# Kernel optimization log

Measured on AMD Instinct MI355X. Metric: run time of the kernel, lower is better.

The kernel has to match this reference:

```python
import jax, jax.numpy as jnp
from jax import lax
import numpy as np

RANK = 128
INPUT_DIM = 128
OUT_DIM = 32
N = 128
L = 512
INIT_STD = 1.0 / np.sqrt(RANK * INPUT_DIM)  # variance-preserving recurrence


def setup_inputs() -> dict:
    key = jax.random.key(0)
    k_x, k_A, k_a, k_O = jax.random.split(key, 4)
    x = jax.random.normal(k_x, (N, L, INPUT_DIM), dtype=jnp.float32)
    A = INIT_STD * jax.random.normal(k_A, (RANK, INPUT_DIM, RANK), dtype=jnp.float32)
    alpha = INIT_STD * jax.random.normal(k_a, (RANK,), dtype=jnp.float32)
    Omega = INIT_STD * jax.random.normal(k_O, (RANK, OUT_DIM), dtype=jnp.float32)
    return {"x": x, "alpha": alpha, "A": A, "Omega": Omega}


def reference(x, alpha, A, Omega):
    # x: [N, L, D]; alpha: [R]; A: [R, D, R]; Omega: [R, M]
    # h_0 = einsum('i,ijk,nj->nk', alpha, A, x[:,0])
    h0 = jnp.einsum('i,ijk,nj->nk', alpha, A, x[:, 0, :])

    def step(h, xt):
        # h: [N, R], xt: [N, D] -> new h: [N, R]
        h = jnp.einsum('ni,ijk,nj->nk', h, A, xt)
        return h, None

    xs = jnp.swapaxes(x, 0, 1)[1:]  # [L-1, N, D]
    h, _ = lax.scan(step, h0, xs)
    out = jnp.einsum('ni,im->nm', h, Omega)  # [N, M]
    return jnp.squeeze(out)
```

## Files before the change

kernel.cpp:

```cpp
#include <hip/hip_runtime.h>

typedef _Float16 f16;
typedef _Float16 half8 __attribute__((ext_vector_type(8)));
typedef _Float16 half4v __attribute__((ext_vector_type(4)));
typedef float f32x4 __attribute__((ext_vector_type(4)));


__global__ void k_cvt_x(const float* __restrict__ in, f16* __restrict__ out) {
    int idx = blockIdx.x * blockDim.x + threadIdx.x;
    float4 v = ((const float4*)in)[idx];
    half4v o;
    o[0] = (f16)v.x; o[1] = (f16)v.y; o[2] = (f16)v.z; o[3] = (f16)v.w;
    ((half4v*)out)[idx] = o;
}

__global__ void k_cvt_A(const float* __restrict__ A, f16* __restrict__ Af2) {
    int o = blockIdx.x * blockDim.x + threadIdx.x;
    int i = o >> 14;
    int k = (o >> 7) & 127;
    int j = o & 127;
    Af2[o] = (f16)A[(i << 14) + (j << 7) + k];
}

__global__ __launch_bounds__(256, 2)
void k_gemm(const f16* __restrict__ Af2, const f16* __restrict__ Xh,
            f16* __restrict__ B, int t0, int logTc) {
    __shared__ f16 lA[128 * 128];
    __shared__ f16 lX[128 * 128];
    const int qtile = blockIdx.x;
    const int i = blockIdx.y;
    const int tid = threadIdx.x;
    const int row = tid >> 4;
    const int ch = tid & 15;
    const int Tcm1 = (1 << logTc) - 1;

    {
        const f16* srcA = Af2 + ((size_t)i << 14);
#pragma unroll
        for (int r = 0; r < 128; r += 16) {
            int rr = row + r;
            uint4 v = *(const uint4*)(srcA + (rr << 7) + (ch << 3));
            *(uint4*)(&lA[(rr << 7) + ((ch ^ (rr & 15)) << 3)]) = v;
        }
#pragma unroll
        for (int r = 0; r < 128; r += 16) {
            int rr = row + r;
            int qr = (qtile << 7) + rr;
            int n = qr >> logTc;
            int trel = qr & Tcm1;
            const f16* srcX = Xh + (((size_t)(n << 9) + t0 + trel) << 7);
            uint4 v = *(const uint4*)(srcX + (ch << 3));
            *(uint4*)(&lX[(rr << 7) + ((ch ^ (rr & 15)) << 3)]) = v;
        }
    }
    __syncthreads();

    const int wave = tid >> 6;
    const int lane = tid & 63;
    const int l15 = lane & 15;
    const int l4 = lane >> 4;
    f32x4 acc[8][2] = {};

#pragma unroll
    for (int ks = 0; ks < 4; ++ks) {
        const int c = (ks << 2) + l4;
        half8 afr[8], bfr[2];
#pragma unroll
        for (int mt = 0; mt < 8; ++mt) {
            int rowA = (mt << 4) + l15;
            afr[mt] = *(const half8*)(&lA[(rowA << 7) + ((c ^ l15) << 3)]);
        }
#pragma unroll
        for (int qt = 0; qt < 2; ++qt) {
            int rowX = (wave << 5) + (qt << 4) + l15;
            bfr[qt] = *(const half8*)(&lX[(rowX << 7) + ((c ^ l15) << 3)]);
        }
#pragma unroll
        for (int mt = 0; mt < 8; ++mt)
#pragma unroll
            for (int qt = 0; qt < 2; ++qt)
                acc[mt][qt] = __builtin_amdgcn_mfma_f32_16x16x32_f16(
                    afr[mt], bfr[qt], acc[mt][qt], 0, 0, 0);
    }

    __syncthreads();
    f16* stage = lA;
#pragma unroll
    for (int mt = 0; mt < 8; ++mt)
#pragma unroll
        for (int qt = 0; qt < 2; ++qt) {
            int q = (wave << 5) + (qt << 4) + l15;
            int chunk = (mt << 1) + (l4 >> 1);
            int hf = l4 & 1;
            half4v o;
            o[0] = (f16)acc[mt][qt][0];
            o[1] = (f16)acc[mt][qt][1];
            o[2] = (f16)acc[mt][qt][2];
            o[3] = (f16)acc[mt][qt][3];
            *(half4v*)(&stage[(q << 7) + (((chunk ^ l15) << 3) + (hf << 2))]) = o;
        }
    __syncthreads();
    {
        const int lr = lane >> 4;
        const int lc = lane & 15;
#pragma unroll
        for (int it = 0; it < 8; ++it) {
            int q = (wave << 5) + (it << 2) + lr;
            uint4 v = *(const uint4*)(&stage[(q << 7) + ((lc ^ (q & 15)) << 3)]);
            size_t qg = (size_t)((qtile << 7) + q);
            *(uint4*)(B + (qg << 14) + (i << 7) + (lc << 3)) = v;
        }
    }
}

__global__ __launch_bounds__(256, 1)
void k_chain(const f16* __restrict__ B, float* __restrict__ hstate,
             const float* __restrict__ alpha, const float* __restrict__ Om,
             float* __restrict__ out, int Tc, int first, int last) {
    __shared__ float hl[128];
    __shared__ float part[16][132];
    const int n = blockIdx.x;
    const int tid = threadIdx.x;
    const int kg = tid & 15;
    const int iq = tid >> 4;

    if (tid < 128) hl[tid] = first ? alpha[tid] : hstate[(n << 7) + tid];
    __syncthreads();

    const f16* bbase = B + (((size_t)n * Tc) << 14) + (iq << 10) + (kg << 3);
    half8 buf[4][8];
#pragma unroll
    for (int s = 0; s < 4; ++s)
#pragma unroll
        for (int ii = 0; ii < 8; ++ii)
            buf[s][ii] = *(const half8*)(bbase + ((size_t)s << 14) + (ii << 7));

    for (int t = 0; t < Tc; t += 4) {
#pragma unroll
        for (int s = 0; s < 4; ++s) {
            float4 h0 = *(const float4*)&hl[iq << 3];
            float4 h1 = *(const float4*)&hl[(iq << 3) + 4];
            float acc[8] = {0, 0, 0, 0, 0, 0, 0, 0};
#pragma unroll
            for (int ii = 0; ii < 4; ++ii) {
                float hv = (&h0.x)[ii];
#pragma unroll
                for (int j = 0; j < 8; ++j)
                    acc[j] += hv * (float)buf[s][ii][j];
            }
#pragma unroll
            for (int ii = 0; ii < 4; ++ii) {
                float hv = (&h1.x)[ii];
#pragma unroll
                for (int j = 0; j < 8; ++j)
                    acc[j] += hv * (float)buf[s][ii + 4][j];
            }
            int tn = t + s + 4;
            if (tn < Tc) {
#pragma unroll
                for (int ii = 0; ii < 8; ++ii)
                    buf[s][ii] = *(const half8*)(bbase + ((size_t)tn << 14) + (ii << 7));
            }
            *(float4*)(&part[iq][kg << 3])       = make_float4(acc[0], acc[1], acc[2], acc[3]);
            *(float4*)(&part[iq][(kg << 3) + 4]) = make_float4(acc[4], acc[5], acc[6], acc[7]);
            __syncthreads();
            if (tid < 128) {
                float s0 = part[0][tid] + part[1][tid];
                float s1 = part[2][tid] + part[3][tid];
                float s2 = part[4][tid] + part[5][tid];
                float s3 = part[6][tid] + part[7][tid];
                s0 += part[8][tid] + part[9][tid];
                s1 += part[10][tid] + part[11][tid];
                s2 += part[12][tid] + part[13][tid];
                s3 += part[14][tid] + part[15][tid];
                hl[tid] = (s0 + s1) + (s2 + s3);
            }
            __syncthreads();
        }
    }

    if (!last) {
        if (tid < 128) hstate[(n << 7) + tid] = hl[tid];
    } else if (tid < 32) {
        float s = 0.f;
        for (int i2 = 0; i2 < 128; ++i2) s += hl[i2] * Om[(i2 << 5) + tid];
        out[(n << 5) + tid] = s;
    }
}

extern "C" void kernel_launch(void* const* d_in, const int* in_sizes, int n_in,
                              void* d_out, int out_size, void* d_ws, size_t ws_size,
                              hipStream_t stream) {
    const float* x     = (const float*)d_in[0];
    const float* alpha = (const float*)d_in[1];
    const float* A     = (const float*)d_in[2];
    const float* Om    = (const float*)d_in[3];
    float* out = (float*)d_out;

    char* ws = (char*)d_ws;
    f16*   Af2    = (f16*)ws;
    f16*   Xh     = (f16*)(ws + ((size_t)4 << 20));
    float* hstate = (float*)(ws + ((size_t)20 << 20));
    f16*   Bc     = (f16*)(ws + ((size_t)21 << 20));

    int Tc = 32;
    while (Tc > 4 && ((size_t)21 << 20) + ((size_t)Tc << 22) > ws_size) Tc >>= 1;
    int logTc = 31 - __builtin_clz(Tc);
    int nch = 512 / Tc;

    k_cvt_x<<<8192, 256, 0, stream>>>(x, Xh);
    k_cvt_A<<<8192, 256, 0, stream>>>(A, Af2);

    for (int c = 0; c < nch; ++c) {
        k_gemm<<<dim3(Tc, 128), 256, 0, stream>>>(Af2, Xh, Bc, c * Tc, logTc);
        k_chain<<<128, 256, 0, stream>>>(Bc, hstate, alpha, Om, out,
                                         Tc, c == 0, c == nch - 1);
    }
    (void)in_sizes; (void)n_in; (void)out_size;
}
```

Measured before the change: 1.017 ms.

## Make GEMM blocks persistent over q-tiles, reusing A slice and prefetching X

The GEMM grid drops from Tc*128 blocks to 512 fixed blocks. Each block loads its A slice into LDS once and loops over Tc/4 q-tiles. The X tile for the next iteration is prefetched into registers while the current MFMA and store phase runs, and the staging buffer moves from lA to lX so A stays resident. This cuts redundant A loads and hides X load latency, at the cost of fewer blocks, more barriers per block, and extra register pressure from the prefetch buffer.

```diff
diff --git a/kernel.cpp b/kernel.cpp
--- a/kernel.cpp
+++ b/kernel.cpp
@@ -24,11 +24,12 @@
 
 __global__ __launch_bounds__(256, 2)
 void k_gemm(const f16* __restrict__ Af2, const f16* __restrict__ Xh,
-            f16* __restrict__ B, int t0, int logTc) {
+            f16* __restrict__ B, int t0, int logTc, int qtPerBlock) {
     __shared__ f16 lA[128 * 128];
     __shared__ f16 lX[128 * 128];
-    const int qtile = blockIdx.x;
-    const int i = blockIdx.y;
+    const int bx = blockIdx.x;
+    const int i = bx >> 2;
+    const int qt0 = bx & 3;
     const int tid = threadIdx.x;
     const int row = tid >> 4;
     const int ch = tid & 15;
@@ -42,74 +43,94 @@
             uint4 v = *(const uint4*)(srcA + (rr << 7) + (ch << 3));
             *(uint4*)(&lA[(rr << 7) + ((ch ^ (rr & 15)) << 3)]) = v;
         }
-#pragma unroll
-        for (int r = 0; r < 128; r += 16) {
-            int rr = row + r;
+    }
+
+    uint4 xr[8];
+    auto loadX = [&](int qtile) {
+#pragma unroll
+        for (int r = 0; r < 8; ++r) {
+            int rr = (r << 4) + row;
             int qr = (qtile << 7) + rr;
             int n = qr >> logTc;
             int trel = qr & Tcm1;
-            const f16* srcX = Xh + (((size_t)(n << 9) + t0 + trel) << 7);
-            uint4 v = *(const uint4*)(srcX + (ch << 3));
-            *(uint4*)(&lX[(rr << 7) + ((ch ^ (rr & 15)) << 3)]) = v;
-        }
-    }
+            xr[r] = *(const uint4*)(Xh + (((size_t)(n << 9) + t0 + trel) << 7) + (ch << 3));
+        }
+    };
+    auto xToLds = [&]() {
+#pragma unroll
+        for (int r = 0; r < 8; ++r) {
+            int rr = (r << 4) + row;
+            *(uint4*)(&lX[(rr << 7) + ((ch ^ (rr & 15)) << 3)]) = xr[r];
+        }
+    };
+
+    loadX(qt0);
+    xToLds();
     __syncthreads();
 
     const int wave = tid >> 6;
     const int lane = tid & 63;
     const int l15 = lane & 15;
     const int l4 = lane >> 4;
-    f32x4 acc[8][2] = {};
-
-#pragma unroll
-    for (int ks = 0; ks < 4; ++ks) {
-        const int c = (ks << 2) + l4;
-        half8 afr[8], bfr[2];
-#pragma unroll
-        for (int mt = 0; mt < 8; ++mt) {
-            int rowA = (mt << 4) + l15;
-            afr[mt] = *(const half8*)(&lA[(rowA << 7) + ((c ^ l15) << 3)]);
-        }
-#pragma unroll
-        for (int qt = 0; qt < 2; ++qt) {
-            int rowX = (wave << 5) + (qt << 4) + l15;
-            bfr[qt] = *(const half8*)(&lX[(rowX << 7) + ((c ^ l15) << 3)]);
-        }
+
+    for (int s = 0; s < qtPerBlock; ++s) {
+        const int qtile = qt0 + (s << 2);
+        const int qtileN = (s + 1 < qtPerBlock) ? qt0 + ((s + 1) << 2) : qt0;
+        loadX(qtileN);
+
+        f32x4 acc[8][2] = {};
+#pragma unroll
+        for (int ks = 0; ks < 4; ++ks) {
+            const int c = (ks << 2) + l4;
+            half8 afr[8], bfr[2];
+#pragma unroll
+            for (int mt = 0; mt < 8; ++mt) {
+                int rowA = (mt << 4) + l15;
+                afr[mt] = *(const half8*)(&lA[(rowA << 7) + ((c ^ l15) << 3)]);
+            }
+#pragma unroll
+            for (int qt = 0; qt < 2; ++qt) {
+                int rowX = (wave << 5) + (qt << 4) + l15;
+                bfr[qt] = *(const half8*)(&lX[(rowX << 7) + ((c ^ l15) << 3)]);
+            }
+#pragma unroll
+            for (int mt = 0; mt < 8; ++mt)
+#pragma unroll
+                for (int qt = 0; qt < 2; ++qt)
+                    acc[mt][qt] = __builtin_amdgcn_mfma_f32_16x16x32_f16(
+                        afr[mt], bfr[qt], acc[mt][qt], 0, 0, 0);
+        }
+
+        __syncthreads();
 #pragma unroll
         for (int mt = 0; mt < 8; ++mt)
 #pragma unroll
-            for (int qt = 0; qt < 2; ++qt)
-                acc[mt][qt] = __builtin_amdgcn_mfma_f32_16x16x32_f16(
-                    afr[mt], bfr[qt], acc[mt][qt], 0, 0, 0);
-    }
-
-    __syncthreads();
-    f16* stage = lA;
-#pragma unroll
-    for (int mt = 0; mt < 8; ++mt)
-#pragma unroll
-        for (int qt = 0; qt < 2; ++qt) {
-            int q = (wave << 5) + (qt << 4) + l15;
-            int chunk = (mt << 1) + (l4 >> 1);
-            int hf = l4 & 1;
-            half4v o;
-            o[0] = (f16)acc[mt][qt][0];
-            o[1] = (f16)acc[mt][qt][1];
-            o[2] = (f16)acc[mt][qt][2];
-            o[3] = (f16)acc[mt][qt][3];
-            *(half4v*)(&stage[(q << 7) + (((chunk ^ l15) << 3) + (hf << 2))]) = o;
-        }
-    __syncthreads();
-    {
-        const int lr = lane >> 4;
-        const int lc = lane & 15;
-#pragma unroll
-        for (int it = 0; it < 8; ++it) {
-            int q = (wave << 5) + (it << 2) + lr;
-            uint4 v = *(const uint4*)(&stage[(q << 7) + ((lc ^ (q & 15)) << 3)]);
-            size_t qg = (size_t)((qtile << 7) + q);
-            *(uint4*)(B + (qg << 14) + (i << 7) + (lc << 3)) = v;
-        }
+            for (int qt = 0; qt < 2; ++qt) {
+                int q = (wave << 5) + (qt << 4) + l15;
+                int chunk = (mt << 1) + (l4 >> 1);
+                int hf = l4 & 1;
+                half4v o;
+                o[0] = (f16)acc[mt][qt][0];
+                o[1] = (f16)acc[mt][qt][1];
+                o[2] = (f16)acc[mt][qt][2];
+                o[3] = (f16)acc[mt][qt][3];
+                *(half4v*)(&lX[(q << 7) + (((chunk ^ l15) << 3) + (hf << 2))]) = o;
+            }
+        __syncthreads();
+        {
+            const int lr = lane >> 4;
+            const int lc = lane & 15;
+#pragma unroll
+            for (int it = 0; it < 8; ++it) {
+                int q = (wave << 5) + (it << 2) + lr;
+                uint4 v = *(const uint4*)(&lX[(q << 7) + ((lc ^ (q & 15)) << 3)]);
+                size_t qg = (size_t)((qtile << 7) + q);
+                *(uint4*)(B + (qg << 14) + (i << 7) + (lc << 3)) = v;
+            }
+        }
+        __syncthreads();
+        xToLds();
+        __syncthreads();
     }
 }
 
@@ -207,12 +228,13 @@
     while (Tc > 4 && ((size_t)21 << 20) + ((size_t)Tc << 22) > ws_size) Tc >>= 1;
     int logTc = 31 - __builtin_clz(Tc);
     int nch = 512 / Tc;
+    int qtPerBlock = Tc / 4;
 
     k_cvt_x<<<8192, 256, 0, stream>>>(x, Xh);
     k_cvt_A<<<8192, 256, 0, stream>>>(A, Af2);
 
     for (int c = 0; c < nch; ++c) {
-        k_gemm<<<dim3(Tc, 128), 256, 0, stream>>>(Af2, Xh, Bc, c * Tc, logTc);
+        k_gemm<<<512, 256, 0, stream>>>(Af2, Xh, Bc, c * Tc, logTc, qtPerBlock);
         k_chain<<<128, 256, 0, stream>>>(Bc, hstate, alpha, Om, out,
                                          Tc, c == 0, c == nch - 1);
     }
```

Measured after the change: 1.414 ms. 39.1% more time.

## Overlap next-chunk GEMM with current chain via fused kernel and double-buffered B

Applied to the files above, without the earlier changes.

Merges the per-chunk GEMM and the sequential chain into one launch. The first 128 blocks run the recurrence chain on the current chunk's B buffer while the remaining blocks compute the next chunk's B into a second buffer. The goal is to hide the GEMM time behind the latency-bound chain and to cut the number of launches. In exchange, the chunk size drops from 32 to 16, which doubles the chunk count, and chain blocks share CUs with GEMM blocks, which can slow the critical chain path.

```diff
diff --git a/kernel.cpp b/kernel.cpp
--- a/kernel.cpp
+++ b/kernel.cpp
@@ -22,14 +22,9 @@
     Af2[o] = (f16)A[(i << 14) + (j << 7) + k];
 }
 
-__global__ __launch_bounds__(256, 2)
-void k_gemm(const f16* __restrict__ Af2, const f16* __restrict__ Xh,
-            f16* __restrict__ B, int t0, int logTc) {
-    __shared__ f16 lA[128 * 128];
-    __shared__ f16 lX[128 * 128];
-    const int qtile = blockIdx.x;
-    const int i = blockIdx.y;
-    const int tid = threadIdx.x;
+__device__ __forceinline__
+void gemm_body(f16* lA, f16* lX, const f16* __restrict__ Af2, const f16* __restrict__ Xh,
+               f16* __restrict__ B, int t0, int logTc, int qtile, int i, int tid) {
     const int row = tid >> 4;
     const int ch = tid & 15;
     const int Tcm1 = (1 << logTc) - 1;
@@ -113,14 +108,11 @@
     }
 }
 
-__global__ __launch_bounds__(256, 1)
-void k_chain(const f16* __restrict__ B, float* __restrict__ hstate,
-             const float* __restrict__ alpha, const float* __restrict__ Om,
-             float* __restrict__ out, int Tc, int first, int last) {
-    __shared__ float hl[128];
-    __shared__ float part[16][132];
-    const int n = blockIdx.x;
-    const int tid = threadIdx.x;
+__device__ __forceinline__
+void chain_body(float* hl, float (*part)[132], const f16* __restrict__ B,
+                float* __restrict__ hstate, const float* __restrict__ alpha,
+                const float* __restrict__ Om, float* __restrict__ out,
+                int Tc, int first, int last, int n, int tid) {
     const int kg = tid & 15;
     const int iq = tid >> 4;
 
@@ -188,6 +180,43 @@
     }
 }
 
+__global__ __launch_bounds__(256, 2)
+void k_gemm(const f16* __restrict__ Af2, const f16* __restrict__ Xh,
+            f16* __restrict__ B, int t0, int logTc) {
+    __shared__ __align__(16) char smem[65536];
+    gemm_body((f16*)smem, (f16*)(smem + 32768), Af2, Xh, B, t0, logTc,
+              blockIdx.x, blockIdx.y, threadIdx.x);
+}
+
+__global__ __launch_bounds__(256, 2)
+void k_chain(const f16* __restrict__ B, float* __restrict__ hstate,
+             const float* __restrict__ alpha, const float* __restrict__ Om,
+             float* __restrict__ out, int Tc, int first, int last) {
+    __shared__ __align__(16) char smem[16384];
+    chain_body((float*)smem, (float(*)[132])(smem + 512), B, hstate, alpha, Om, out,
+               Tc, first, last, blockIdx.x, threadIdx.x);
+}
+
+__global__ __launch_bounds__(256, 2)
+void k_fused(const f16* __restrict__ Af2, const f16* __restrict__ Xh,
+             f16* __restrict__ Bw, const f16* __restrict__ Br,
+             float* __restrict__ hstate, const float* __restrict__ alpha,
+             const float* __restrict__ Om, float* __restrict__ out,
+             int t0g, int logTc, int Tc, int first, int last) {
+    __shared__ __align__(16) char smem[65536];
+    const int bx = blockIdx.x;
+    if (bx < 128) {
+        chain_body((float*)smem, (float(*)[132])(smem + 512), Br, hstate, alpha, Om, out,
+                   Tc, first, last, bx, threadIdx.x);
+    } else {
+        int g = bx - 128;
+        int qtile = g & (Tc - 1);
+        int i = g >> logTc;
+        gemm_body((f16*)smem, (f16*)(smem + 32768), Af2, Xh, Bw, t0g, logTc,
+                  qtile, i, threadIdx.x);
+    }
+}
+
 extern "C" void kernel_launch(void* const* d_in, const int* in_sizes, int n_in,
                               void* d_out, int out_size, void* d_ws, size_t ws_size,
                               hipStream_t stream) {
@@ -201,20 +230,30 @@
     f16*   Af2    = (f16*)ws;
     f16*   Xh     = (f16*)(ws + ((size_t)4 << 20));
     float* hstate = (float*)(ws + ((size_t)20 << 20));
-    f16*   Bc     = (f16*)(ws + ((size_t)21 << 20));
-
-    int Tc = 32;
-    while (Tc > 4 && ((size_t)21 << 20) + ((size_t)Tc << 22) > ws_size) Tc >>= 1;
+
+    int Tc = 16;
+    while (Tc > 4 && ((size_t)21 << 20) + (((size_t)Tc << 22) * 2) > ws_size) Tc >>= 1;
     int logTc = 31 - __builtin_clz(Tc);
     int nch = 512 / Tc;
+    f16* Bc[2];
+    Bc[0] = (f16*)(ws + ((size_t)21 << 20));
+    Bc[1] = (f16*)(ws + ((size_t)21 << 20) + ((size_t)Tc << 22));
 
     k_cvt_x<<<8192, 256, 0, stream>>>(x, Xh);
     k_cvt_A<<<8192, 256, 0, stream>>>(A, Af2);
 
+    k_gemm<<<dim3(Tc, 128), 256, 0, stream>>>(Af2, Xh, Bc[0], 0, logTc);
+
     for (int c = 0; c < nch; ++c) {
-        k_gemm<<<dim3(Tc, 128), 256, 0, stream>>>(Af2, Xh, Bc, c * Tc, logTc);
-        k_chain<<<128, 256, 0, stream>>>(Bc, hstate, alpha, Om, out,
-                                         Tc, c == 0, c == nch - 1);
+        const f16* br = Bc[c & 1];
+        if (c + 1 < nch) {
+            k_fused<<<128 + Tc * 128, 256, 0, stream>>>(
+                Af2, Xh, Bc[(c + 1) & 1], br, hstate, alpha, Om, out,
+                (c + 1) * Tc, logTc, Tc, c == 0, c == nch - 1);
+        } else {
+            k_chain<<<128, 256, 0, stream>>>(br, hstate, alpha, Om, out,
+                                             Tc, c == 0, c == nch - 1);
+        }
     }
     (void)in_sizes; (void)n_in; (void)out_size;
 }
```

After: 966.4 us. -5.0%, faster.
